# Kernel optimization log

Hardware: AMD Instinct MI355X
Metric: run time of the kernel (lower is better)

The kernel has to match this reference:

```python
import jax, jax.numpy as jnp
import numpy as np

N_HEADS = 16
MAX_LEN = 1024


def setup_inputs() -> dict:
    key = jax.random.key(0)
    ks = jax.random.split(key, 6)
    B, T, C = 4, 1024, 1024
    scale = 0.02
    return {
        "x": jax.random.normal(ks[0], (B, T, C), dtype=jnp.float32),
        "qkv_w": jax.random.normal(ks[1], (3 * C, C), dtype=jnp.float32) * scale,
        "qkv_b": jax.random.normal(ks[2], (3 * C,), dtype=jnp.float32) * scale,
        "proj_w": jax.random.normal(ks[3], (C, C), dtype=jnp.float32) * scale,
        "proj_b": jax.random.normal(ks[4], (C,), dtype=jnp.float32) * scale,
        "rel_pos_emb": jax.random.normal(ks[5], (2 * MAX_LEN - 1, C), dtype=jnp.float32) * scale,
    }


def reference(x, qkv_w, qkv_b, proj_w, proj_b, rel_pos_emb):
    B, T, C = x.shape
    H = N_HEADS
    D = C // H
    # QKV projection: (B,T,3C) -> (3,B,H,T,D)
    qkv = (x @ qkv_w.T + qkv_b).reshape(B, T, 3, H, D)
    qkv = jnp.transpose(qkv, (2, 0, 3, 1, 4))
    q, k, v = qkv[0], qkv[1], qkv[2]
    # scores: (B,H,T,T)
    att = jnp.einsum("bhtd,bhsd->bhts", q, k) / np.sqrt(D).astype(np.float32)
    # Relative position bias: gather-then-sum == sum-then-gather over head_dim.
    # Pre-reduce table to (2*max_len-1, H) to avoid materializing (T,T,C).
    table = rel_pos_emb.reshape(2 * MAX_LEN - 1, H, D).sum(axis=-1)  # (2L-1, H)
    pos = jnp.arange(T)
    rel_idx = pos[:, None] - pos[None, :] + (MAX_LEN - 1)  # (T,T)
    bias = jnp.transpose(table[rel_idx], (2, 0, 1))  # (H,T,T)
    att = att + bias[None]
    # causal mask: positions j > i masked to -inf
    causal = pos[None, :] > pos[:, None]  # (T,T) True above diagonal
    att = jnp.where(causal[None, None], -jnp.inf, att)
    att = jax.nn.softmax(att, axis=-1)
    out = jnp.einsum("bhts,bhsd->bhtd", att, v)  # (B,H,T,D)
    out = jnp.transpose(out, (0, 2, 1, 3)).reshape(B, T, C)
    return out @ proj_w.T + proj_b
```

## Files before the change

kernel.cpp:

```cpp
#include <hip/hip_runtime.h>
#include <hip/hip_bf16.h>
#include <cstdint>


typedef __bf16 bf16x8 __attribute__((ext_vector_type(8)));
typedef float f32x4 __attribute__((ext_vector_type(4)));
typedef float f32x16 __attribute__((ext_vector_type(16)));

__device__ __forceinline__ float bf2f(unsigned short u) {
    return __uint_as_float(((unsigned)u) << 16);
}
__device__ __forceinline__ unsigned short f2bf(float f) {
    __hip_bfloat16 h = __float2bfloat16(f);
    return *reinterpret_cast<unsigned short*>(&h);
}
__device__ __forceinline__ unsigned pk2(float a, float b) {
    return (unsigned)f2bf(a) | ((unsigned)f2bf(b) << 16);
}
__device__ __forceinline__ int4 cvt8(float4 a, float4 b) {
    union { unsigned short s[8]; int4 v; } u;
    u.s[0] = f2bf(a.x); u.s[1] = f2bf(a.y); u.s[2] = f2bf(a.z); u.s[3] = f2bf(a.w);
    u.s[4] = f2bf(b.x); u.s[5] = f2bf(b.y); u.s[6] = f2bf(b.z); u.s[7] = f2bf(b.w);
    return u.v;
}

__device__ __forceinline__ void gload16(const void* g, void* l) {
    __builtin_amdgcn_global_load_lds(
        reinterpret_cast<const __attribute__((address_space(1))) unsigned int*>(
            reinterpret_cast<uintptr_t>(g)),
        reinterpret_cast<__attribute__((address_space(3))) unsigned int*>(
            reinterpret_cast<uintptr_t>(l)),
        16, 0, 0);
}

__global__ __launch_bounds__(256) void cvt3(const float* __restrict__ x,
                                            const float* __restrict__ w1,
                                            const float* __restrict__ w2,
                                            unsigned short* __restrict__ ox,
                                            unsigned short* __restrict__ ow1,
                                            unsigned short* __restrict__ ow2) {
    const int i = blockIdx.x * 256 + threadIdx.x;
    const float* s; unsigned short* d; int li;
    if (i < 524288)      { s = x;  d = ox;  li = i; }
    else if (i < 917504) { s = w1; d = ow1; li = i - 524288; }
    else                 { s = w2; d = ow2; li = i - 917504; }
    const float4 a = *(const float4*)(s + (size_t)li * 8);
    const float4 b = *(const float4*)(s + (size_t)li * 8 + 4);
    *(int4*)(d + (size_t)li * 8) = cvt8(a, b);
}

__global__ __launch_bounds__(1024) void table_reduce(const float* __restrict__ rel,
                                                     float* __restrict__ table) {
    const int p = blockIdx.x;
    const int w = threadIdx.x >> 6, lane = threadIdx.x & 63;
    float v = rel[(size_t)p * 1024 + w * 64 + lane];
#pragma unroll
    for (int o = 32; o; o >>= 1) v += __shfl_xor(v, o, 64);
    if (lane == 0) table[p * 16 + w] = v;
}

template <int EPI>
__global__ __launch_bounds__(512) void gemm_bt(const unsigned short* __restrict__ A,
                                               const unsigned short* __restrict__ B,
                                               const float* __restrict__ bias,
                                               unsigned short* __restrict__ outb,
                                               float* __restrict__ outf,
                                               int M, int N, int K) {
    __shared__ __attribute__((aligned(16))) unsigned short As[128 * 32];
    __shared__ __attribute__((aligned(16))) unsigned short Bs[128 * 32];
    const int bm = blockIdx.x * 128, bn = blockIdx.y * 128;
    const int tid = threadIdx.x, lane = tid & 63, wave = tid >> 6;
    const int wr = wave & 1, wc = wave >> 1;
    const int quad = lane >> 4, lm = lane & 15;

    const int srow = tid >> 2;
    const int scol = (tid & 3) * 8;
    const unsigned short* Ap = A + (size_t)(bm + srow) * K + scol;
    const unsigned short* Bp = B + (size_t)(bn + srow) * K + scol;
    unsigned short* AsW = &As[tid * 8];
    unsigned short* BsW = &Bs[tid * 8];

    f32x4 acc[4][2];
#pragma unroll
    for (int r = 0; r < 4; ++r)
#pragma unroll
        for (int c = 0; c < 2; ++c) acc[r][c] = (f32x4){0.f, 0.f, 0.f, 0.f};

    for (int kk = 0; kk < K; kk += 32) {
        gload16(Ap + kk, AsW);
        gload16(Bp + kk, BsW);
        __syncthreads();

        bf16x8 af[4], bfr[2];
#pragma unroll
        for (int r = 0; r < 4; ++r)
            af[r] = *(const bf16x8*)(&As[(64 * wr + 16 * r + lm) * 32 + quad * 8]);
#pragma unroll
        for (int c = 0; c < 2; ++c)
            bfr[c] = *(const bf16x8*)(&Bs[(32 * wc + 16 * c + lm) * 32 + quad * 8]);
#pragma unroll
        for (int r = 0; r < 4; ++r)
#pragma unroll
            for (int c = 0; c < 2; ++c)
                acc[r][c] = __builtin_amdgcn_mfma_f32_16x16x32_bf16(af[r], bfr[c], acc[r][c], 0, 0, 0);
        __syncthreads();
    }

#pragma unroll
    for (int r = 0; r < 4; ++r)
#pragma unroll
        for (int c = 0; c < 2; ++c)
#pragma unroll
            for (int i = 0; i < 4; ++i) {
                const int row = bm + 64 * wr + 16 * r + quad * 4 + i;
                const int col = bn + 32 * wc + 16 * c + lm;
                const float v = acc[r][c][i] + bias[col];
                if (EPI == 0) {
                    const int b = row >> 10, t = row & 1023;
                    const int s3 = col >> 10, rem = col & 1023;
                    const int h = rem >> 6, d = rem & 63;
                    const size_t base = (((size_t)s3 * 4 + b) * 16 + h) * 65536;
                    const size_t off = base + (s3 == 2 ? (size_t)d * 1024 + t
                                                       : (size_t)t * 64 + d);
                    outb[off] = f2bf(v);
                } else {
                    outf[(size_t)row * N + col] = v;
                }
            }
}

#define LOADK(DST, KT)                                                        \
    do {                                                                      \
        const unsigned short* kr_ = Kg + (size_t)((KT) * 32 + l5) * 64 + hi8; \
        DST[0] = *(const bf16x8*)(kr_);                                       \
        DST[1] = *(const bf16x8*)(kr_ + 16);                                  \
        DST[2] = *(const bf16x8*)(kr_ + 32);                                  \
        DST[3] = *(const bf16x8*)(kr_ + 48);                                  \
    } while (0)

#define ATTN_TILE(KF, KT)                                                     \
    do {                                                                      \
        const int jb = (KT) * 32;                                             \
        const unsigned short* vb_ = Vtg + (size_t)l5 * 1024 + jb + hi8;       \
        const bf16x8 vf00 = *(const bf16x8*)(vb_);                            \
        const bf16x8 vf01 = *(const bf16x8*)(vb_ + 16);                       \
        const bf16x8 vf10 = *(const bf16x8*)(vb_ + 32768);                    \
        const bf16x8 vf11 = *(const bf16x8*)(vb_ + 32768 + 16);               \
        f32x16 s = {0.f};                                                     \
        _Pragma("unroll")                                                     \
        for (int t = 0; t < 4; ++t)                                           \
            s = __builtin_amdgcn_mfma_f32_32x32x16_bf16(KF[t], qf[t], s, 0, 0, 0); \
        float p[16];                                                          \
        _Pragma("unroll")                                                     \
        for (int reg = 0; reg < 16; ++reg) {                                  \
            const int j = jb + (reg & 3) + 8 * (reg >> 2) + 4 * hi;           \
            p[reg] = fmaf(s[reg], 0.125f, tb[q - j + 127]);                   \
        }                                                                     \
        if (jb + 31 > qbase) {                                                \
            _Pragma("unroll")                                                 \
            for (int reg = 0; reg < 16; ++reg) {                              \
                const int j = jb + (reg & 3) + 8 * (reg >> 2) + 4 * hi;       \
                p[reg] = (j <= q) ? p[reg] : -1e30f;                          \
            }                                                                 \
        }                                                                     \
        float mx = p[0];                                                      \
        _Pragma("unroll")                                                     \
        for (int reg = 1; reg < 16; ++reg) mx = fmaxf(mx, p[reg]);            \
        mx = fmaxf(mx, __shfl_xor(mx, 32, 64));                               \
        if (!__all(mx <= mi + 8.f)) {                                         \
            const float mnew = fmaxf(mi, mx);                                 \
            const float alpha = __expf(mi - mnew);                            \
            mi = mnew;                                                        \
            li *= alpha;                                                      \
            _Pragma("unroll")                                                 \
            for (int reg = 0; reg < 16; ++reg) {                              \
                oa0[reg] *= alpha;                                            \
                oa1[reg] *= alpha;                                            \
            }                                                                 \
        }                                                                     \
        float lsum = 0.f;                                                     \
        _Pragma("unroll")                                                     \
        for (int reg = 0; reg < 16; ++reg) {                                  \
            p[reg] = __expf(p[reg] - mi);                                     \
            lsum += p[reg];                                                   \
        }                                                                     \
        li += lsum;                                                           \
        const unsigned P0 = pk2(p[0], p[1]),   P1 = pk2(p[2], p[3]);          \
        const unsigned P2 = pk2(p[4], p[5]),   P3 = pk2(p[6], p[7]);          \
        const unsigned P4 = pk2(p[8], p[9]),   P5 = pk2(p[10], p[11]);        \
        const unsigned P6 = pk2(p[12], p[13]), P7 = pk2(p[14], p[15]);        \
        const unsigned R0 = __shfl_xor(hi ? P0 : P2, 32, 64);                 \
        const unsigned R1 = __shfl_xor(hi ? P1 : P3, 32, 64);                 \
        const unsigned R2 = __shfl_xor(hi ? P4 : P6, 32, 64);                 \
        const unsigned R3 = __shfl_xor(hi ? P5 : P7, 32, 64);                 \
        union { unsigned w[4]; bf16x8 v; } bq0, bq1;                          \
        bq0.w[0] = hi ? R0 : P0;  bq0.w[1] = hi ? R1 : P1;                    \
        bq0.w[2] = hi ? P2 : R0;  bq0.w[3] = hi ? P3 : R1;                    \
        bq1.w[0] = hi ? R2 : P4;  bq1.w[1] = hi ? R3 : P5;                    \
        bq1.w[2] = hi ? P6 : R2;  bq1.w[3] = hi ? P7 : R3;                    \
        oa0 = __builtin_amdgcn_mfma_f32_32x32x16_bf16(vf00, bq0.v, oa0, 0, 0, 0); \
        oa0 = __builtin_amdgcn_mfma_f32_32x32x16_bf16(vf01, bq1.v, oa0, 0, 0, 0); \
        oa1 = __builtin_amdgcn_mfma_f32_32x32x16_bf16(vf10, bq0.v, oa1, 0, 0, 0); \
        oa1 = __builtin_amdgcn_mfma_f32_32x32x16_bf16(vf11, bq1.v, oa1, 0, 0, 0); \
    } while (0)

#define PACKP(p, BQA, BQB)                                                    \
    do {                                                                      \
        const unsigned P0 = pk2(p[0], p[1]),   P1 = pk2(p[2], p[3]);          \
        const unsigned P2 = pk2(p[4], p[5]),   P3 = pk2(p[6], p[7]);          \
        const unsigned P4 = pk2(p[8], p[9]),   P5 = pk2(p[10], p[11]);        \
        const unsigned P6 = pk2(p[12], p[13]), P7 = pk2(p[14], p[15]);        \
        const unsigned R0 = __shfl_xor(hi ? P0 : P2, 32, 64);                 \
        const unsigned R1 = __shfl_xor(hi ? P1 : P3, 32, 64);                 \
        const unsigned R2 = __shfl_xor(hi ? P4 : P6, 32, 64);                 \
        const unsigned R3 = __shfl_xor(hi ? P5 : P7, 32, 64);                 \
        BQA.w[0] = hi ? R0 : P0;  BQA.w[1] = hi ? R1 : P1;                    \
        BQA.w[2] = hi ? P2 : R0;  BQA.w[3] = hi ? P3 : R1;                    \
        BQB.w[0] = hi ? R2 : P4;  BQB.w[1] = hi ? R3 : P5;                    \
        BQB.w[2] = hi ? P6 : R2;  BQB.w[3] = hi ? P7 : R3;                    \
    } while (0)

#define ATTN_TILE2(KT)                                                        \
    do {                                                                      \
        const int jb = (KT) * 32;                                             \
        const unsigned short* vb_ = Vtg + (size_t)l5 * 1024 + jb + hi8;       \
        const bf16x8 vf00 = *(const bf16x8*)(vb_);                            \
        const bf16x8 vf01 = *(const bf16x8*)(vb_ + 16);                       \
        const bf16x8 vf02 = *(const bf16x8*)(vb_ + 32);                       \
        const bf16x8 vf03 = *(const bf16x8*)(vb_ + 48);                       \
        const bf16x8 vf10 = *(const bf16x8*)(vb_ + 32768);                    \
        const bf16x8 vf11 = *(const bf16x8*)(vb_ + 32768 + 16);               \
        const bf16x8 vf12 = *(const bf16x8*)(vb_ + 32768 + 32);               \
        const bf16x8 vf13 = *(const bf16x8*)(vb_ + 32768 + 48);               \
        f32x16 s0v = {0.f}, s1v = {0.f};                                      \
        _Pragma("unroll")                                                     \
        for (int t = 0; t < 4; ++t) {                                         \
            s0v = __builtin_amdgcn_mfma_f32_32x32x16_bf16(kA[t], qf[t], s0v, 0, 0, 0); \
            s1v = __builtin_amdgcn_mfma_f32_32x32x16_bf16(kB[t], qf[t], s1v, 0, 0, 0); \
        }                                                                     \
        if ((KT) + 2 < nt) LOADK(kA, (KT) + 2);                               \
        if ((KT) + 3 < nt) LOADK(kB, (KT) + 3);                               \
        float p0[16], p1[16];                                                 \
        _Pragma("unroll")                                                     \
        for (int reg = 0; reg < 16; ++reg) {                                  \
            const int jo = (reg & 3) + 8 * (reg >> 2) + 4 * hi;               \
            p0[reg] = fmaf(s0v[reg], 0.125f, tb[q - jb - jo + 127]);          \
            p1[reg] = fmaf(s1v[reg], 0.125f, tb[q - jb - 32 - jo + 127]);     \
        }                                                                     \
        if (jb + 63 > qbase) {                                                \
            _Pragma("unroll")                                                 \
            for (int reg = 0; reg < 16; ++reg) {                              \
                const int jo = (reg & 3) + 8 * (reg >> 2) + 4 * hi;           \
                p0[reg] = (jb + jo <= q) ? p0[reg] : -1e30f;                  \
                p1[reg] = (jb + 32 + jo <= q) ? p1[reg] : -1e30f;             \
            }                                                                 \
        }                                                                     \
        float mx = p0[0];                                                     \
        _Pragma("unroll")                                                     \
        for (int reg = 1; reg < 16; ++reg) mx = fmaxf(mx, p0[reg]);           \
        _Pragma("unroll")                                                     \
        for (int reg = 0; reg < 16; ++reg) mx = fmaxf(mx, p1[reg]);           \
        mx = fmaxf(mx, __shfl_xor(mx, 32, 64));                               \
        if (!__all(mx <= mi + 8.f)) {                                         \
            const float mnew = fmaxf(mi, mx);                                 \
            const float alpha = __expf(mi - mnew);                            \
            mi = mnew;                                                        \
            li *= alpha;                                                      \
            _Pragma("unroll")                                                 \
            for (int reg = 0; reg < 16; ++reg) {                              \
                oa0[reg] *= alpha;                                            \
                oa1[reg] *= alpha;                                            \
            }                                                                 \
        }                                                                     \
        float lsum = 0.f;                                                     \
        _Pragma("unroll")                                                     \
        for (int reg = 0; reg < 16; ++reg) {                                  \
            p0[reg] = __expf(p0[reg] - mi);                                   \
            p1[reg] = __expf(p1[reg] - mi);                                   \
            lsum += p0[reg] + p1[reg];                                        \
        }                                                                     \
        li += lsum;                                                           \
        union { unsigned w[4]; bf16x8 v; } bq00, bq01, bq10, bq11;            \
        PACKP(p0, bq00, bq01);                                                \
        PACKP(p1, bq10, bq11);                                                \
        oa0 = __builtin_amdgcn_mfma_f32_32x32x16_bf16(vf00, bq00.v, oa0, 0, 0, 0); \
        oa1 = __builtin_amdgcn_mfma_f32_32x32x16_bf16(vf10, bq00.v, oa1, 0, 0, 0); \
        oa0 = __builtin_amdgcn_mfma_f32_32x32x16_bf16(vf01, bq01.v, oa0, 0, 0, 0); \
        oa1 = __builtin_amdgcn_mfma_f32_32x32x16_bf16(vf11, bq01.v, oa1, 0, 0, 0); \
        oa0 = __builtin_amdgcn_mfma_f32_32x32x16_bf16(vf02, bq10.v, oa0, 0, 0, 0); \
        oa1 = __builtin_amdgcn_mfma_f32_32x32x16_bf16(vf12, bq10.v, oa1, 0, 0, 0); \
        oa0 = __builtin_amdgcn_mfma_f32_32x32x16_bf16(vf03, bq11.v, oa0, 0, 0, 0); \
        oa1 = __builtin_amdgcn_mfma_f32_32x32x16_bf16(vf13, bq11.v, oa1, 0, 0, 0); \
    } while (0)

__global__ __launch_bounds__(128) void attn_mfma(const unsigned short* __restrict__ qkvb,
                                                 const float* __restrict__ table,
                                                 unsigned short* __restrict__ y) {
    const int bh = blockIdx.x, b = bh >> 4, h = bh & 15;
    const int level = 15 - blockIdx.y;
    const int tid = threadIdx.x, lane = tid & 63, wave = tid >> 6;
    const int l5 = lane & 31, hi = lane >> 5, hi8 = hi * 8;

    __shared__ float tb[1152];

    const unsigned short* Qg  = qkvb + ((size_t)(b)*16 + h) * 65536;
    const unsigned short* Kg  = qkvb + ((size_t)(4 + b)*16 + h) * 65536;
    const unsigned short* Vtg = qkvb + ((size_t)(8 + b)*16 + h) * 65536;

    const int qbase = 64 * level + 32 * wave;
    const int q = qbase + l5;
    const int nt = 2 * level + wave + 1;

    bf16x8 qf[4];
    {
        const unsigned short* qr = Qg + (size_t)q * 64 + hi8;
#pragma unroll
        for (int t = 0; t < 4; ++t) qf[t] = *(const bf16x8*)(qr + t * 16);
    }

    const int tbn = 64 * level + 191;
    for (int i = tid; i < tbn; i += 128) tb[i] = table[(896 + i) * 16 + h];
    __syncthreads();

    f32x16 oa0 = {0.f}, oa1 = {0.f};
    float mi = -1e30f, li = 0.f;

    bf16x8 kA[4], kB[4];
    LOADK(kA, 0);
    LOADK(kB, nt > 1 ? 1 : 0);
    int kt = 0;
    for (; kt + 1 < nt; kt += 2) ATTN_TILE2(kt);
    if (kt < nt) ATTN_TILE(kA, kt);

    li += __shfl_xor(li, 32, 64);
    const float linv = 1.0f / li;
    unsigned short* yq = y + ((size_t)(b * 1024 + q)) * 1024 + h * 64;
#pragma unroll
    for (int g = 0; g < 4; ++g) {
        union { unsigned short u[4]; int2 v; } o4a, o4b;
#pragma unroll
        for (int i = 0; i < 4; ++i) {
            o4a.u[i] = f2bf(oa0[4 * g + i] * linv);
            o4b.u[i] = f2bf(oa1[4 * g + i] * linv);
        }
        *(int2*)(yq + 8 * g + 4 * hi) = o4a.v;
        *(int2*)(yq + 32 + 8 * g + 4 * hi) = o4b.v;
    }
}

extern "C" void kernel_launch(void* const* d_in, const int* in_sizes, int n_in,
                              void* d_out, int out_size, void* d_ws, size_t ws_size,
                              hipStream_t stream) {
    const float* x      = (const float*)d_in[0];
    const float* qkv_w  = (const float*)d_in[1];
    const float* qkv_b  = (const float*)d_in[2];
    const float* proj_w = (const float*)d_in[3];
    const float* proj_b = (const float*)d_in[4];
    const float* rel    = (const float*)d_in[5];
    float* out = (float*)d_out;

    char* ws = (char*)d_ws;
    unsigned short* xb   = (unsigned short*)(ws + 0);
    unsigned short* qwb  = (unsigned short*)(ws + 8388608);
    unsigned short* pwb  = (unsigned short*)(ws + 14680064);
    float* table         = (float*)(ws + 16777216);
    unsigned short* qkvb = (unsigned short*)(ws + 16908288);
    unsigned short* yb   = (unsigned short*)(ws + 42074112);

    cvt3<<<4096, 256, 0, stream>>>(x, qkv_w, proj_w, xb, qwb, pwb);
    table_reduce<<<2047, 1024, 0, stream>>>(rel, table);
    gemm_bt<0><<<dim3(32, 24), 512, 0, stream>>>(xb, qwb, qkv_b, qkvb, nullptr,
                                                 4096, 3072, 1024);
    attn_mfma<<<dim3(64, 16), 128, 0, stream>>>(qkvb, table, yb);
    gemm_bt<1><<<dim3(32, 8), 512, 0, stream>>>(yb, pwb, proj_b, nullptr, out,
                                                4096, 1024, 1024);
}
```

Baseline: 193.2 us.

## Split attention KV range across four waves with LDS softmax merge

Each attention block now covers a single 32-row query tile and splits that tile's causal key range across four waves (split-K flash attention). At the end the partial max, sum and output accumulators are merged through shared memory and written by one wave. The goal is to balance the causal work and raise parallelism, since the grid doubles to 64x32 blocks of 256 threads. In exchange it adds LDS traffic, a block barrier, a serial merge on one wave, and redundant Q loads and table staging per block.

Measured after the change: 215.9 us. +11.8%, slower.

```diff
diff --git a/kernel.cpp b/kernel.cpp
--- a/kernel.cpp
+++ b/kernel.cpp
@@ -238,8 +238,8 @@
             s0v = __builtin_amdgcn_mfma_f32_32x32x16_bf16(kA[t], qf[t], s0v, 0, 0, 0); \
             s1v = __builtin_amdgcn_mfma_f32_32x32x16_bf16(kB[t], qf[t], s1v, 0, 0, 0); \
         }                                                                     \
-        if ((KT) + 2 < nt) LOADK(kA, (KT) + 2);                               \
-        if ((KT) + 3 < nt) LOADK(kB, (KT) + 3);                               \
+        if ((KT) + 2 < kend) LOADK(kA, (KT) + 2);                             \
+        if ((KT) + 3 < kend) LOADK(kB, (KT) + 3);                             \
         float p0[16], p1[16];                                                 \
         _Pragma("unroll")                                                     \
         for (int reg = 0; reg < 16; ++reg) {                                  \
@@ -293,23 +293,28 @@
         oa1 = __builtin_amdgcn_mfma_f32_32x32x16_bf16(vf13, bq11.v, oa1, 0, 0, 0); \
     } while (0)
 
-__global__ __launch_bounds__(128) void attn_mfma(const unsigned short* __restrict__ qkvb,
+__global__ __launch_bounds__(256) void attn_mfma(const unsigned short* __restrict__ qkvb,
                                                  const float* __restrict__ table,
                                                  unsigned short* __restrict__ y) {
     const int bh = blockIdx.x, b = bh >> 4, h = bh & 15;
-    const int level = 15 - blockIdx.y;
+    const int s = 31 - blockIdx.y;
     const int tid = threadIdx.x, lane = tid & 63, wave = tid >> 6;
     const int l5 = lane & 31, hi = lane >> 5, hi8 = hi * 8;
 
     __shared__ float tb[1152];
+    __shared__ float mls[3][2][64];
+    __shared__ __attribute__((aligned(16))) float oas[3][64][32];
 
     const unsigned short* Qg  = qkvb + ((size_t)(b)*16 + h) * 65536;
     const unsigned short* Kg  = qkvb + ((size_t)(4 + b)*16 + h) * 65536;
     const unsigned short* Vtg = qkvb + ((size_t)(8 + b)*16 + h) * 65536;
 
-    const int qbase = 64 * level + 32 * wave;
+    const int qbase = 32 * s;
     const int q = qbase + l5;
-    const int nt = 2 * level + wave + 1;
+    const int nt = s + 1;
+    const int nch = (nt + 3) >> 2;
+    const int ks = wave * nch;
+    const int kend = (ks + nch < nt) ? ks + nch : nt;
 
     bf16x8 qf[4];
     {
@@ -318,33 +323,61 @@
         for (int t = 0; t < 4; ++t) qf[t] = *(const bf16x8*)(qr + t * 16);
     }
 
-    const int tbn = 64 * level + 191;
-    for (int i = tid; i < tbn; i += 128) tb[i] = table[(896 + i) * 16 + h];
+    const int tbn = 32 * s + 159;
+    for (int i = tid; i < tbn; i += 256) tb[i] = table[(896 + i) * 16 + h];
     __syncthreads();
 
     f32x16 oa0 = {0.f}, oa1 = {0.f};
     float mi = -1e30f, li = 0.f;
 
-    bf16x8 kA[4], kB[4];
-    LOADK(kA, 0);
-    LOADK(kB, nt > 1 ? 1 : 0);
-    int kt = 0;
-    for (; kt + 1 < nt; kt += 2) ATTN_TILE2(kt);
-    if (kt < nt) ATTN_TILE(kA, kt);
-
-    li += __shfl_xor(li, 32, 64);
-    const float linv = 1.0f / li;
-    unsigned short* yq = y + ((size_t)(b * 1024 + q)) * 1024 + h * 64;
-#pragma unroll
-    for (int g = 0; g < 4; ++g) {
-        union { unsigned short u[4]; int2 v; } o4a, o4b;
-#pragma unroll
-        for (int i = 0; i < 4; ++i) {
-            o4a.u[i] = f2bf(oa0[4 * g + i] * linv);
-            o4b.u[i] = f2bf(oa1[4 * g + i] * linv);
+    if (ks < kend) {
+        bf16x8 kA[4], kB[4];
+        LOADK(kA, ks);
+        LOADK(kB, (kend - ks > 1) ? ks + 1 : ks);
+        int kt = ks;
+        for (; kt + 1 < kend; kt += 2) ATTN_TILE2(kt);
+        if (kt < kend) ATTN_TILE(kA, kt);
+    }
+
+    if (wave < 3) {
+        mls[wave][0][lane] = mi;
+        mls[wave][1][lane] = li;
+#pragma unroll
+        for (int r = 0; r < 16; ++r) {
+            oas[wave][lane][r] = oa0[r];
+            oas[wave][lane][16 + r] = oa1[r];
         }
-        *(int2*)(yq + 8 * g + 4 * hi) = o4a.v;
-        *(int2*)(yq + 32 + 8 * g + 4 * hi) = o4b.v;
+    }
+    __syncthreads();
+    if (wave == 3) {
+        const float m0 = mls[0][0][lane], m1 = mls[1][0][lane], m2 = mls[2][0][lane];
+        const float mstar = fmaxf(fmaxf(m0, m1), fmaxf(m2, mi));
+        const float w0 = __expf(m0 - mstar), w1 = __expf(m1 - mstar);
+        const float w2 = __expf(m2 - mstar), w3 = __expf(mi - mstar);
+        float lm = w0 * mls[0][1][lane] + w1 * mls[1][1][lane] +
+                   w2 * mls[2][1][lane] + w3 * li;
+        f32x16 O0, O1;
+#pragma unroll
+        for (int r = 0; r < 16; ++r) {
+            O0[r] = w0 * oas[0][lane][r] + w1 * oas[1][lane][r] +
+                    w2 * oas[2][lane][r] + w3 * oa0[r];
+            O1[r] = w0 * oas[0][lane][16 + r] + w1 * oas[1][lane][16 + r] +
+                    w2 * oas[2][lane][16 + r] + w3 * oa1[r];
+        }
+        lm += __shfl_xor(lm, 32, 64);
+        const float linv = 1.0f / lm;
+        unsigned short* yq = y + ((size_t)(b * 1024 + q)) * 1024 + h * 64;
+#pragma unroll
+        for (int g = 0; g < 4; ++g) {
+            union { unsigned short u[4]; int2 v; } o4a, o4b;
+#pragma unroll
+            for (int i = 0; i < 4; ++i) {
+                o4a.u[i] = f2bf(O0[4 * g + i] * linv);
+                o4b.u[i] = f2bf(O1[4 * g + i] * linv);
+            }
+            *(int2*)(yq + 8 * g + 4 * hi) = o4a.v;
+            *(int2*)(yq + 32 + 8 * g + 4 * hi) = o4b.v;
+        }
     }
 }
 
@@ -371,7 +404,7 @@
     table_reduce<<<2047, 1024, 0, stream>>>(rel, table);
     gemm_bt<0><<<dim3(32, 24), 512, 0, stream>>>(xb, qwb, qkv_b, qkvb, nullptr,
                                                  4096, 3072, 1024);
-    attn_mfma<<<dim3(64, 16), 128, 0, stream>>>(qkvb, table, yb);
+    attn_mfma<<<dim3(64, 32), 256, 0, stream>>>(qkvb, table, yb);
     gemm_bt<1><<<dim3(32, 8), 512, 0, stream>>>(yb, pwb, proj_b, nullptr, out,
                                                 4096, 1024, 1024);
 }
```

## Double-buffer GEMM shared tiles and use permlane32 swap for P packing

Applied to the files above, without the earlier changes.

The bf16 GEMM main loop now uses two LDS buffers, so the async global-to-LDS load of the next K slice is issued before the MFMAs on the current slice. This aims to overlap load latency with compute and halves the barrier count per K step, at the cost of doubling LDS usage. Separately, the attention P-matrix repacking replaces four ds_bpermute-style shuffles plus selects with v_permlane32_swap_b32, which exchanges register halves between the two 32-lane halves directly.

Result: no change. 193.2 us (+0.0%).

```diff
diff --git a/kernel.cpp b/kernel.cpp
--- a/kernel.cpp
+++ b/kernel.cpp
@@ -59,6 +59,22 @@
     if (lane == 0) table[p * 16 + w] = v;
 }
 
+#define GSTEP(AS_, BS_)                                                       \
+    do {                                                                      \
+        bf16x8 af[4], bfr[2];                                                 \
+        _Pragma("unroll")                                                     \
+        for (int r = 0; r < 4; ++r)                                           \
+            af[r] = *(const bf16x8*)(&AS_[(64 * wr + 16 * r + lm) * 32 + quad * 8]); \
+        _Pragma("unroll")                                                     \
+        for (int c = 0; c < 2; ++c)                                           \
+            bfr[c] = *(const bf16x8*)(&BS_[(32 * wc + 16 * c + lm) * 32 + quad * 8]); \
+        _Pragma("unroll")                                                     \
+        for (int r = 0; r < 4; ++r)                                           \
+            _Pragma("unroll")                                                 \
+            for (int c = 0; c < 2; ++c)                                       \
+                acc[r][c] = __builtin_amdgcn_mfma_f32_16x16x32_bf16(af[r], bfr[c], acc[r][c], 0, 0, 0); \
+    } while (0)
+
 template <int EPI>
 __global__ __launch_bounds__(512) void gemm_bt(const unsigned short* __restrict__ A,
                                                const unsigned short* __restrict__ B,
@@ -66,8 +82,10 @@
                                                unsigned short* __restrict__ outb,
                                                float* __restrict__ outf,
                                                int M, int N, int K) {
-    __shared__ __attribute__((aligned(16))) unsigned short As[128 * 32];
-    __shared__ __attribute__((aligned(16))) unsigned short Bs[128 * 32];
+    __shared__ __attribute__((aligned(16))) unsigned short As0[128 * 32];
+    __shared__ __attribute__((aligned(16))) unsigned short Bs0[128 * 32];
+    __shared__ __attribute__((aligned(16))) unsigned short As1[128 * 32];
+    __shared__ __attribute__((aligned(16))) unsigned short Bs1[128 * 32];
     const int bm = blockIdx.x * 128, bn = blockIdx.y * 128;
     const int tid = threadIdx.x, lane = tid & 63, wave = tid >> 6;
     const int wr = wave & 1, wc = wave >> 1;
@@ -77,8 +95,10 @@
     const int scol = (tid & 3) * 8;
     const unsigned short* Ap = A + (size_t)(bm + srow) * K + scol;
     const unsigned short* Bp = B + (size_t)(bn + srow) * K + scol;
-    unsigned short* AsW = &As[tid * 8];
-    unsigned short* BsW = &Bs[tid * 8];
+    unsigned short* AsW0 = &As0[tid * 8];
+    unsigned short* BsW0 = &Bs0[tid * 8];
+    unsigned short* AsW1 = &As1[tid * 8];
+    unsigned short* BsW1 = &Bs1[tid * 8];
 
     f32x4 acc[4][2];
 #pragma unroll
@@ -86,23 +106,23 @@
 #pragma unroll
         for (int c = 0; c < 2; ++c) acc[r][c] = (f32x4){0.f, 0.f, 0.f, 0.f};
 
-    for (int kk = 0; kk < K; kk += 32) {
-        gload16(Ap + kk, AsW);
-        gload16(Bp + kk, BsW);
+    gload16(Ap, AsW0);
+    gload16(Bp, BsW0);
+    __syncthreads();
+
+    for (int kk = 0; kk < K; kk += 64) {
+        if (kk + 32 < K) {
+            gload16(Ap + kk + 32, AsW1);
+            gload16(Bp + kk + 32, BsW1);
+        }
+        GSTEP(As0, Bs0);
         __syncthreads();
 
-        bf16x8 af[4], bfr[2];
-#pragma unroll
-        for (int r = 0; r < 4; ++r)
-            af[r] = *(const bf16x8*)(&As[(64 * wr + 16 * r + lm) * 32 + quad * 8]);
-#pragma unroll
-        for (int c = 0; c < 2; ++c)
-            bfr[c] = *(const bf16x8*)(&Bs[(32 * wc + 16 * c + lm) * 32 + quad * 8]);
-#pragma unroll
-        for (int r = 0; r < 4; ++r)
-#pragma unroll
-            for (int c = 0; c < 2; ++c)
-                acc[r][c] = __builtin_amdgcn_mfma_f32_16x16x32_bf16(af[r], bfr[c], acc[r][c], 0, 0, 0);
+        if (kk + 64 < K) {
+            gload16(Ap + kk + 64, AsW0);
+            gload16(Bp + kk + 64, BsW0);
+        }
+        GSTEP(As1, Bs1);
         __syncthreads();
     }
 
@@ -138,6 +158,20 @@
         DST[3] = *(const bf16x8*)(kr_ + 48);                                  \
     } while (0)
 
+#define PACKP(p, BQA, BQB)                                                    \
+    do {                                                                      \
+        unsigned Q0 = pk2(p[0], p[1]),   Q1 = pk2(p[2], p[3]);                \
+        unsigned Q2 = pk2(p[4], p[5]),   Q3 = pk2(p[6], p[7]);                \
+        unsigned Q4 = pk2(p[8], p[9]),   Q5 = pk2(p[10], p[11]);              \
+        unsigned Q6 = pk2(p[12], p[13]), Q7 = pk2(p[14], p[15]);              \
+        asm volatile("v_permlane32_swap_b32 %0, %1" : "+v"(Q0), "+v"(Q2));    \
+        asm volatile("v_permlane32_swap_b32 %0, %1" : "+v"(Q1), "+v"(Q3));    \
+        asm volatile("v_permlane32_swap_b32 %0, %1" : "+v"(Q4), "+v"(Q6));    \
+        asm volatile("v_permlane32_swap_b32 %0, %1" : "+v"(Q5), "+v"(Q7));    \
+        BQA.w[0] = Q0;  BQA.w[1] = Q1;  BQA.w[2] = Q2;  BQA.w[3] = Q3;        \
+        BQB.w[0] = Q4;  BQB.w[1] = Q5;  BQB.w[2] = Q6;  BQB.w[3] = Q7;        \
+    } while (0)
+
 #define ATTN_TILE(KF, KT)                                                     \
     do {                                                                      \
         const int jb = (KT) * 32;                                             \
@@ -185,39 +219,12 @@
             lsum += p[reg];                                                   \
         }                                                                     \
         li += lsum;                                                           \
-        const unsigned P0 = pk2(p[0], p[1]),   P1 = pk2(p[2], p[3]);          \
-        const unsigned P2 = pk2(p[4], p[5]),   P3 = pk2(p[6], p[7]);          \
-        const unsigned P4 = pk2(p[8], p[9]),   P5 = pk2(p[10], p[11]);        \
-        const unsigned P6 = pk2(p[12], p[13]), P7 = pk2(p[14], p[15]);        \
-        const unsigned R0 = __shfl_xor(hi ? P0 : P2, 32, 64);                 \
-        const unsigned R1 = __shfl_xor(hi ? P1 : P3, 32, 64);                 \
-        const unsigned R2 = __shfl_xor(hi ? P4 : P6, 32, 64);                 \
-        const unsigned R3 = __shfl_xor(hi ? P5 : P7, 32, 64);                 \
         union { unsigned w[4]; bf16x8 v; } bq0, bq1;                          \
-        bq0.w[0] = hi ? R0 : P0;  bq0.w[1] = hi ? R1 : P1;                    \
-        bq0.w[2] = hi ? P2 : R0;  bq0.w[3] = hi ? P3 : R1;                    \
-        bq1.w[0] = hi ? R2 : P4;  bq1.w[1] = hi ? R3 : P5;                    \
-        bq1.w[2] = hi ? P6 : R2;  bq1.w[3] = hi ? P7 : R3;                    \
+        PACKP(p, bq0, bq1);                                                   \
         oa0 = __builtin_amdgcn_mfma_f32_32x32x16_bf16(vf00, bq0.v, oa0, 0, 0, 0); \
         oa0 = __builtin_amdgcn_mfma_f32_32x32x16_bf16(vf01, bq1.v, oa0, 0, 0, 0); \
         oa1 = __builtin_amdgcn_mfma_f32_32x32x16_bf16(vf10, bq0.v, oa1, 0, 0, 0); \
         oa1 = __builtin_amdgcn_mfma_f32_32x32x16_bf16(vf11, bq1.v, oa1, 0, 0, 0); \
-    } while (0)
-
-#define PACKP(p, BQA, BQB)                                                    \
-    do {                                                                      \
-        const unsigned P0 = pk2(p[0], p[1]),   P1 = pk2(p[2], p[3]);          \
-        const unsigned P2 = pk2(p[4], p[5]),   P3 = pk2(p[6], p[7]);          \
-        const unsigned P4 = pk2(p[8], p[9]),   P5 = pk2(p[10], p[11]);        \
-        const unsigned P6 = pk2(p[12], p[13]), P7 = pk2(p[14], p[15]);        \
-        const unsigned R0 = __shfl_xor(hi ? P0 : P2, 32, 64);                 \
-        const unsigned R1 = __shfl_xor(hi ? P1 : P3, 32, 64);                 \
-        const unsigned R2 = __shfl_xor(hi ? P4 : P6, 32, 64);                 \
-        const unsigned R3 = __shfl_xor(hi ? P5 : P7, 32, 64);                 \
-        BQA.w[0] = hi ? R0 : P0;  BQA.w[1] = hi ? R1 : P1;                    \
-        BQA.w[2] = hi ? P2 : R0;  BQA.w[3] = hi ? P3 : R1;                    \
-        BQB.w[0] = hi ? R2 : P4;  BQB.w[1] = hi ? R3 : P5;                    \
-        BQB.w[2] = hi ? P6 : R2;  BQB.w[3] = hi ? P7 : R3;                    \
     } while (0)
 
 #define ATTN_TILE2(KT)                                                        \
```
